# Kernel optimization log

Measured on AMD Instinct MI355X. Metric: run time of the kernel, lower is better.

## Reference

```python
import jax, jax.numpy as jnp
import numpy as np

IN_DIMS = 1024
OUT_DIMS = 1024
N_TOKENS = 32768


def setup_inputs() -> dict:
    key = jax.random.key(0)
    k_x, k_wl0, k_wl1, k_scale, k_shift, k_noise = jax.random.split(key, 6)
    x = jax.random.normal(k_x, (N_TOKENS, IN_DIMS), dtype=jnp.float32)
    # weight_logits[..., 0]: magnitude logits, weight_logits[..., 1]: sign logits
    gain = np.sqrt(2.0)  # relu gain
    a = gain * np.sqrt(6.0 / (IN_DIMS + OUT_DIMS))
    mag_logits = jax.random.uniform(k_wl0, (OUT_DIMS, IN_DIMS), dtype=jnp.float32,
                                    minval=-a, maxval=a)  # logit(0.5)=0, so centered at 0
    sgn_logits = jax.random.uniform(k_wl1, (OUT_DIMS, IN_DIMS), dtype=jnp.float32,
                                    minval=-a, maxval=a)
    weight_logits = jnp.stack([mag_logits, sgn_logits], axis=-1)  # [O, I, 2]
    scale = jnp.full((OUT_DIMS,), np.float32(a), dtype=jnp.float32)
    shift = jnp.full((OUT_DIMS,), 0.01, dtype=jnp.float32)
    noise = jax.random.normal(k_noise, (N_TOKENS, OUT_DIMS), dtype=jnp.float32)
    return {"x": x, "weight_logits": weight_logits, "scale": scale,
            "shift": shift, "noise": noise}


def reference(x, weight_logits, scale, shift, noise):
    # train_forward of TernaryLinear
    weight_p = jax.nn.sigmoid(weight_logits)          # [O, I, 2]
    p_mag = weight_p[..., 0]                          # P(|w| = 1)
    p_sgn = weight_p[..., 1]                          # P(w > 0 | |w| = 1)
    s = 2.0 * p_sgn - 1.0
    weight_mean = p_mag * s                           # [O, I]
    weight_var = p_mag - (p_mag * p_mag) * (s * s)    # [O, I], >= 0
    out_mean = jnp.einsum('ni,oi->no', x, weight_mean)         # [N, O]
    out_var = jnp.einsum('ni,oi->no', x * x, weight_var)       # [N, O]
    out = out_mean + jnp.sqrt(out_var) * noise
    out = out * scale[None, :] + shift[None, :]
    return out
```

## Files before the change

kernel.cpp:

```cpp
#include <hip/hip_runtime.h>
#include <hip/hip_bf16.h>
#include <cmath>

#define N_TOK 32768
#define KDIM  1024
#define ODIM  1024

#define BM 128
#define BN 128
#define BK 64
#define NKT (KDIM / BK)

typedef float          f32x4  __attribute__((ext_vector_type(4)));
typedef __bf16         bf16x8 __attribute__((ext_vector_type(8)));
typedef unsigned short us8    __attribute__((ext_vector_type(8)));
typedef unsigned short us4    __attribute__((ext_vector_type(4)));
typedef unsigned short us2    __attribute__((ext_vector_type(2)));

static __device__ __forceinline__ unsigned short f2bf(float f) {
  unsigned u = __builtin_bit_cast(unsigned, f);
  u += 0x7FFFu + ((u >> 16) & 1u);
  return (unsigned short)(u >> 16);
}

static __device__ __forceinline__ f32x4 mfma16(us8 a, us8 b, f32x4 c) {
  return __builtin_amdgcn_mfma_f32_16x16x32_bf16(
      __builtin_bit_cast(bf16x8, a), __builtin_bit_cast(bf16x8, b), c, 0, 0, 0);
}

static __device__ __forceinline__ void gl_lds16(const void* g, void* l) {
  __builtin_amdgcn_global_load_lds(
      (const __attribute__((address_space(1))) void*)g,
      (__attribute__((address_space(3))) void*)l, 16, 0, 0);
}

__global__ void wprep_kernel(const float* __restrict__ wl,
                             unsigned short* __restrict__ wm,
                             unsigned short* __restrict__ wv) {
  int i = blockIdx.x * blockDim.x + threadIdx.x;
  f32x4 v = *reinterpret_cast<const f32x4*>(wl + (size_t)i * 4);
  float pm0 = 1.f / (1.f + expf(-v.x));
  float ps0 = 1.f / (1.f + expf(-v.y));
  float pm1 = 1.f / (1.f + expf(-v.z));
  float ps1 = 1.f / (1.f + expf(-v.w));
  float m0 = pm0 * (2.f * ps0 - 1.f);
  float m1 = pm1 * (2.f * ps1 - 1.f);
  float q0 = pm0 - m0 * m0;
  float q1 = pm1 - m1 * m1;
  us2 am = {f2bf(m0), f2bf(m1)};
  us2 av = {f2bf(q0), f2bf(q1)};
  *reinterpret_cast<us2*>(wm + (size_t)i * 2) = am;
  *reinterpret_cast<us2*>(wv + (size_t)i * 2) = av;
}

__global__ __launch_bounds__(256, 2) void ternary_gemm(
    const float* __restrict__ x,
    const unsigned short* __restrict__ wm,
    const unsigned short* __restrict__ wv,
    const float* __restrict__ scale,
    const float* __restrict__ shift,
    const float* __restrict__ noise,
    float* __restrict__ out) {
  __shared__ alignas(16) unsigned short AsX[BM * BK];
  __shared__ alignas(16) unsigned short AsX2[BM * BK];
  __shared__ alignas(16) unsigned short BsM[BN * BK];
  __shared__ alignas(16) unsigned short BsV[BN * BK];

  const int tid  = threadIdx.x;
  const int lane = tid & 63;
  const int w    = tid >> 6;
  const int wr   = w >> 1;
  const int wc   = w & 1;
  const int l15  = lane & 15;
  const int l4   = lane >> 4;

  const int bid = blockIdx.x;
  const int swz = (bid & 7) * 256 + (bid >> 3);
  const int bm  = swz >> 3;
  const int bn  = swz & 7;
  const int rowBase = bm * BM;
  const int colBase = bn * BN;

  f32x4 accM[4][4];
  f32x4 accV[4][4];
#pragma unroll
  for (int i = 0; i < 4; ++i)
#pragma unroll
    for (int j = 0; j < 4; ++j) { accM[i][j] = (f32x4)0.f; accV[i][j] = (f32x4)0.f; }

  const float* xbase = x + (size_t)rowBase * KDIM;

  f32x4 apre[8];
#pragma unroll
  for (int jj = 0; jj < 8; ++jj) {
    int flat = jj * 256 + tid;
    int r    = flat >> 4;
    int c4   = flat & 15;
    apre[jj] = *reinterpret_cast<const f32x4*>(xbase + (size_t)r * KDIM + c4 * 4);
  }

  for (int kt = 0; kt < NKT; ++kt) {
    const int k0 = kt * BK;

#pragma unroll
    for (int r = 0; r < 4; ++r) {
      int issue = w * 4 + r;
      int slot  = issue * 64 + lane;
      int row   = slot >> 3;
      int j     = slot & 7;
      int ke    = (j ^ (row & 7)) << 3;
      size_t goff = (size_t)(colBase + row) * KDIM + k0 + ke;
      gl_lds16(wm + goff, (char*)BsM + issue * 1024);
      gl_lds16(wv + goff, (char*)BsV + issue * 1024);
    }

#pragma unroll
    for (int jj = 0; jj < 8; ++jj) {
      int flat = jj * 256 + tid;
      int r    = flat >> 4;
      int c4   = flat & 15;
      f32x4 vx = apre[jj];
      us4 bx  = {f2bf(vx.x), f2bf(vx.y), f2bf(vx.z), f2bf(vx.w)};
      us4 bx2 = {f2bf(vx.x * vx.x), f2bf(vx.y * vx.y),
                 f2bf(vx.z * vx.z), f2bf(vx.w * vx.w)};
      int off = r * 128 + ((c4 * 8) ^ ((r & 7) << 4));
      *reinterpret_cast<us4*>((char*)AsX + off)  = bx;
      *reinterpret_cast<us4*>((char*)AsX2 + off) = bx2;
    }

    __syncthreads();

    if (kt + 1 < NKT) {
      const float* xnext = xbase + (kt + 1) * BK;
#pragma unroll
      for (int jj = 0; jj < 8; ++jj) {
        int flat = jj * 256 + tid;
        int r    = flat >> 4;
        int c4   = flat & 15;
        apre[jj] = *reinterpret_cast<const f32x4*>(xnext + (size_t)r * KDIM + c4 * 4);
      }
    }

#pragma unroll
    for (int ks = 0; ks < 2; ++ks) {
      us8 ax[4], ax2[4], bmf[4], bvf[4];
      const int kb = ks * 64 + (l4 << 4);
#pragma unroll
      for (int am = 0; am < 4; ++am) {
        int row = wr * 64 + am * 16 + l15;
        int off = row * 128 + (kb ^ ((row & 7) << 4));
        ax[am]  = *reinterpret_cast<const us8*>((const char*)AsX + off);
        ax2[am] = *reinterpret_cast<const us8*>((const char*)AsX2 + off);
      }
#pragma unroll
      for (int b = 0; b < 4; ++b) {
        int row = wc * 64 + b * 16 + l15;
        int off = row * 128 + (kb ^ ((row & 7) << 4));
        bmf[b] = *reinterpret_cast<const us8*>((const char*)BsM + off);
        bvf[b] = *reinterpret_cast<const us8*>((const char*)BsV + off);
      }
#pragma unroll
      for (int am = 0; am < 4; ++am)
#pragma unroll
        for (int b = 0; b < 4; ++b) {
          accM[am][b] = mfma16(ax[am],  bmf[b], accM[am][b]);
          accV[am][b] = mfma16(ax2[am], bvf[b], accV[am][b]);
        }
    }
    __syncthreads();
  }

#pragma unroll
  for (int am = 0; am < 4; ++am) {
    int row0 = rowBase + wr * 64 + am * 16 + (l4 << 2);
#pragma unroll
    for (int b = 0; b < 4; ++b) {
      int col = colBase + wc * 64 + b * 16 + l15;
      float sc = scale[col];
      float sh = shift[col];
#pragma unroll
      for (int j = 0; j < 4; ++j) {
        size_t idx = (size_t)(row0 + j) * ODIM + col;
        float nm = accM[am][b][j];
        float nv = accV[am][b][j];
        float nz = noise[idx];
        out[idx] = fmaf(nm + sqrtf(fmaxf(nv, 0.f)) * nz, sc, sh);
      }
    }
  }
}

extern "C" void kernel_launch(void* const* d_in, const int* in_sizes, int n_in,
                              void* d_out, int out_size, void* d_ws, size_t ws_size,
                              hipStream_t stream) {
  const float* x     = (const float*)d_in[0];
  const float* wl    = (const float*)d_in[1];
  const float* scale = (const float*)d_in[2];
  const float* shift = (const float*)d_in[3];
  const float* noise = (const float*)d_in[4];
  float* out = (float*)d_out;

  unsigned short* wm = (unsigned short*)d_ws;
  unsigned short* wv = wm + (size_t)ODIM * KDIM;

  wprep_kernel<<<(ODIM * KDIM / 2) / 256, 256, 0, stream>>>(wl, wm, wv);

  ternary_gemm<<<(N_TOK / BM) * (ODIM / BN), 256, 0, stream>>>(
      x, wm, wv, scale, shift, noise, out);
}
```

Before: 218.3 us.

## Split mean and variance GEMMs across separate wave groups with LDS exchange epilogue

The block grows to 512 threads. Four waves now compute the mean GEMM and four compute the variance GEMM, so each wave holds half as many accumulators and each tile is loaded with half as many instructions per thread. The epilogue swaps half of each accumulator tile through a padded LDS region that reuses the staging buffers, so both groups write output and share the noise and store work. This also switches to the native bf16 conversion and raises the launch bound to 4 blocks. The risks are the extra LDS exchange and barrier, the larger shared memory footprint (about 66KB) limiting occupancy, and whether the 4-block bound forces register spills.

```diff
diff --git a/kernel.cpp b/kernel.cpp
--- a/kernel.cpp
+++ b/kernel.cpp
@@ -10,11 +10,12 @@
 #define BN 128
 #define BK 64
 #define NKT (KDIM / BK)
+#define THREADS 512
 
 typedef float          f32x4  __attribute__((ext_vector_type(4)));
 typedef __bf16         bf16x8 __attribute__((ext_vector_type(8)));
+typedef __bf16         bf16x4 __attribute__((ext_vector_type(4)));
 typedef unsigned short us8    __attribute__((ext_vector_type(8)));
-typedef unsigned short us4    __attribute__((ext_vector_type(4)));
 typedef unsigned short us2    __attribute__((ext_vector_type(2)));
 
 static __device__ __forceinline__ unsigned short f2bf(float f) {
@@ -53,7 +54,7 @@
   *reinterpret_cast<us2*>(wv + (size_t)i * 2) = av;
 }
 
-__global__ __launch_bounds__(256, 2) void ternary_gemm(
+__global__ __launch_bounds__(THREADS, 4) void ternary_gemm(
     const float* __restrict__ x,
     const unsigned short* __restrict__ wm,
     const unsigned short* __restrict__ wv,
@@ -61,16 +62,21 @@
     const float* __restrict__ shift,
     const float* __restrict__ noise,
     float* __restrict__ out) {
-  __shared__ alignas(16) unsigned short AsX[BM * BK];
-  __shared__ alignas(16) unsigned short AsX2[BM * BK];
-  __shared__ alignas(16) unsigned short BsM[BN * BK];
-  __shared__ alignas(16) unsigned short BsV[BN * BK];
+  __shared__ alignas(16) char smem[67584];
+  unsigned short* AsX  = (unsigned short*)smem;
+  unsigned short* AsX2 = (unsigned short*)(smem + 16384);
+  unsigned short* BsM  = (unsigned short*)(smem + 32768);
+  unsigned short* BsV  = (unsigned short*)(smem + 49152);
+  float* Mex = (float*)smem;
+  float* Vex = ((float*)smem) + 4 * 32 * 66;
 
   const int tid  = threadIdx.x;
   const int lane = tid & 63;
   const int w    = tid >> 6;
-  const int wr   = w >> 1;
-  const int wc   = w & 1;
+  const bool isVar = (w >= 4);
+  const int p    = w & 3;
+  const int wr   = p >> 1;
+  const int wc   = p & 1;
   const int l15  = lane & 15;
   const int l4   = lane >> 4;
 
@@ -81,51 +87,52 @@
   const int rowBase = bm * BM;
   const int colBase = bn * BN;
 
-  f32x4 accM[4][4];
-  f32x4 accV[4][4];
+  f32x4 acc[4][4];
 #pragma unroll
   for (int i = 0; i < 4; ++i)
 #pragma unroll
-    for (int j = 0; j < 4; ++j) { accM[i][j] = (f32x4)0.f; accV[i][j] = (f32x4)0.f; }
+    for (int j = 0; j < 4; ++j) acc[i][j] = (f32x4)0.f;
 
   const float* xbase = x + (size_t)rowBase * KDIM;
 
-  f32x4 apre[8];
-#pragma unroll
-  for (int jj = 0; jj < 8; ++jj) {
-    int flat = jj * 256 + tid;
+  f32x4 apre[4];
+#pragma unroll
+  for (int jj = 0; jj < 4; ++jj) {
+    int flat = jj * THREADS + tid;
     int r    = flat >> 4;
     int c4   = flat & 15;
     apre[jj] = *reinterpret_cast<const f32x4*>(xbase + (size_t)r * KDIM + c4 * 4);
   }
 
+  const char* Abase = isVar ? (const char*)AsX2 : (const char*)AsX;
+  const char* Bbase = isVar ? (const char*)BsV  : (const char*)BsM;
+
   for (int kt = 0; kt < NKT; ++kt) {
     const int k0 = kt * BK;
 
 #pragma unroll
-    for (int r = 0; r < 4; ++r) {
-      int issue = w * 4 + r;
-      int slot  = issue * 64 + lane;
-      int row   = slot >> 3;
-      int j     = slot & 7;
-      int ke    = (j ^ (row & 7)) << 3;
+    for (int r = 0; r < 2; ++r) {
+      int slot = r * THREADS + tid;
+      int row  = slot >> 3;
+      int j    = slot & 7;
+      int ke   = (j ^ (row & 7)) << 3;
       size_t goff = (size_t)(colBase + row) * KDIM + k0 + ke;
-      gl_lds16(wm + goff, (char*)BsM + issue * 1024);
-      gl_lds16(wv + goff, (char*)BsV + issue * 1024);
-    }
-
-#pragma unroll
-    for (int jj = 0; jj < 8; ++jj) {
-      int flat = jj * 256 + tid;
+      gl_lds16(wm + goff, (char*)BsM + slot * 16);
+      gl_lds16(wv + goff, (char*)BsV + slot * 16);
+    }
+
+#pragma unroll
+    for (int jj = 0; jj < 4; ++jj) {
+      int flat = jj * THREADS + tid;
       int r    = flat >> 4;
       int c4   = flat & 15;
       f32x4 vx = apre[jj];
-      us4 bx  = {f2bf(vx.x), f2bf(vx.y), f2bf(vx.z), f2bf(vx.w)};
-      us4 bx2 = {f2bf(vx.x * vx.x), f2bf(vx.y * vx.y),
-                 f2bf(vx.z * vx.z), f2bf(vx.w * vx.w)};
+      bf16x4 bx  = {(__bf16)vx.x, (__bf16)vx.y, (__bf16)vx.z, (__bf16)vx.w};
+      bf16x4 bx2 = {(__bf16)(vx.x * vx.x), (__bf16)(vx.y * vx.y),
+                    (__bf16)(vx.z * vx.z), (__bf16)(vx.w * vx.w)};
       int off = r * 128 + ((c4 * 8) ^ ((r & 7) << 4));
-      *reinterpret_cast<us4*>((char*)AsX + off)  = bx;
-      *reinterpret_cast<us4*>((char*)AsX2 + off) = bx2;
+      *reinterpret_cast<bf16x4*>((char*)AsX + off)  = bx;
+      *reinterpret_cast<bf16x4*>((char*)AsX2 + off) = bx2;
     }
 
     __syncthreads();
@@ -133,8 +140,8 @@
     if (kt + 1 < NKT) {
       const float* xnext = xbase + (kt + 1) * BK;
 #pragma unroll
-      for (int jj = 0; jj < 8; ++jj) {
-        int flat = jj * 256 + tid;
+      for (int jj = 0; jj < 4; ++jj) {
+        int flat = jj * THREADS + tid;
         int r    = flat >> 4;
         int c4   = flat & 15;
         apre[jj] = *reinterpret_cast<const f32x4*>(xnext + (size_t)r * KDIM + c4 * 4);
@@ -143,50 +150,86 @@
 
 #pragma unroll
     for (int ks = 0; ks < 2; ++ks) {
-      us8 ax[4], ax2[4], bmf[4], bvf[4];
+      us8 af[4], bf_[4];
       const int kb = ks * 64 + (l4 << 4);
 #pragma unroll
       for (int am = 0; am < 4; ++am) {
         int row = wr * 64 + am * 16 + l15;
         int off = row * 128 + (kb ^ ((row & 7) << 4));
-        ax[am]  = *reinterpret_cast<const us8*>((const char*)AsX + off);
-        ax2[am] = *reinterpret_cast<const us8*>((const char*)AsX2 + off);
+        af[am] = *reinterpret_cast<const us8*>(Abase + off);
       }
 #pragma unroll
       for (int b = 0; b < 4; ++b) {
         int row = wc * 64 + b * 16 + l15;
         int off = row * 128 + (kb ^ ((row & 7) << 4));
-        bmf[b] = *reinterpret_cast<const us8*>((const char*)BsM + off);
-        bvf[b] = *reinterpret_cast<const us8*>((const char*)BsV + off);
+        bf_[b] = *reinterpret_cast<const us8*>(Bbase + off);
       }
 #pragma unroll
       for (int am = 0; am < 4; ++am)
 #pragma unroll
-        for (int b = 0; b < 4; ++b) {
-          accM[am][b] = mfma16(ax[am],  bmf[b], accM[am][b]);
-          accV[am][b] = mfma16(ax2[am], bvf[b], accV[am][b]);
-        }
+        for (int b = 0; b < 4; ++b)
+          acc[am][b] = mfma16(af[am], bf_[b], acc[am][b]);
     }
     __syncthreads();
   }
 
-#pragma unroll
-  for (int am = 0; am < 4; ++am) {
-    int row0 = rowBase + wr * 64 + am * 16 + (l4 << 2);
-#pragma unroll
-    for (int b = 0; b < 4; ++b) {
-      int col = colBase + wc * 64 + b * 16 + l15;
-      float sc = scale[col];
-      float sh = shift[col];
-#pragma unroll
-      for (int j = 0; j < 4; ++j) {
-        size_t idx = (size_t)(row0 + j) * ODIM + col;
-        float nm = accM[am][b][j];
-        float nv = accV[am][b][j];
-        float nz = noise[idx];
-        out[idx] = fmaf(nm + sqrtf(fmaxf(nv, 0.f)) * nz, sc, sh);
-      }
-    }
+  if (!isVar) {
+#pragma unroll
+    for (int am = 2; am < 4; ++am)
+#pragma unroll
+      for (int b = 0; b < 4; ++b)
+#pragma unroll
+        for (int j = 0; j < 4; ++j) {
+          int lr = am * 16 + l4 * 4 + j;
+          int lc = b * 16 + l15;
+          Mex[(p * 32 + (lr - 32)) * 66 + lc] = acc[am][b][j];
+        }
+  } else {
+#pragma unroll
+    for (int am = 0; am < 2; ++am)
+#pragma unroll
+      for (int b = 0; b < 4; ++b)
+#pragma unroll
+        for (int j = 0; j < 4; ++j) {
+          int lr = am * 16 + l4 * 4 + j;
+          int lc = b * 16 + l15;
+          Vex[(p * 32 + lr) * 66 + lc] = acc[am][b][j];
+        }
+  }
+  __syncthreads();
+
+  if (!isVar) {
+#pragma unroll
+    for (int am = 0; am < 2; ++am)
+#pragma unroll
+      for (int b = 0; b < 4; ++b) {
+        int col = colBase + wc * 64 + b * 16 + l15;
+        float sc = scale[col];
+        float sh = shift[col];
+#pragma unroll
+        for (int j = 0; j < 4; ++j) {
+          int lr = am * 16 + l4 * 4 + j;
+          float vv = Vex[(p * 32 + lr) * 66 + b * 16 + l15];
+          size_t idx = (size_t)(rowBase + wr * 64 + lr) * ODIM + col;
+          out[idx] = fmaf(acc[am][b][j] + sqrtf(fmaxf(vv, 0.f)) * noise[idx], sc, sh);
+        }
+      }
+  } else {
+#pragma unroll
+    for (int am = 2; am < 4; ++am)
+#pragma unroll
+      for (int b = 0; b < 4; ++b) {
+        int col = colBase + wc * 64 + b * 16 + l15;
+        float sc = scale[col];
+        float sh = shift[col];
+#pragma unroll
+        for (int j = 0; j < 4; ++j) {
+          int lr = am * 16 + l4 * 4 + j;
+          float mm = Mex[(p * 32 + (lr - 32)) * 66 + b * 16 + l15];
+          size_t idx = (size_t)(rowBase + wr * 64 + lr) * ODIM + col;
+          out[idx] = fmaf(mm + sqrtf(fmaxf(acc[am][b][j], 0.f)) * noise[idx], sc, sh);
+        }
+      }
   }
 }
 
@@ -205,6 +248,6 @@
 
   wprep_kernel<<<(ODIM * KDIM / 2) / 256, 256, 0, stream>>>(wl, wm, wv);
 
-  ternary_gemm<<<(N_TOK / BM) * (ODIM / BN), 256, 0, stream>>>(
+  ternary_gemm<<<(N_TOK / BM) * (ODIM / BN), THREADS, 0, stream>>>(
       x, wm, wv, scale, shift, noise, out);
 }
```

After: 207.9 us. 1.05x faster.
